# Kernel optimization log

Measured on AMD Instinct MI355X. Metric: run time of the kernel, lower is better.

The kernel has to match this reference:

```python
import jax, jax.numpy as jnp
import numpy as np

B, L, R, E, D = 16, 28, 64, 34, 512


def setup_inputs() -> dict:
    key = jax.random.key(0)
    ks = jax.random.split(key, 10)
    logits = jax.random.uniform(ks[0], (B, L, R), dtype=jnp.float32)
    evt_embeddings = jax.random.normal(ks[1], (B, 1, D), dtype=jnp.float32)
    arg_embeddings = jax.random.normal(ks[2], (B, L, D), dtype=jnp.float32)
    # valid-arg counts in [1, L] (used as mask-count multiplier and divisor)
    arg_padding_num = jax.random.randint(ks[3], (B,), 1, L + 1).astype(jnp.float32)
    evt_type_list = jax.random.randint(ks[4], (B,), 0, E)
    s = 1.0 / np.sqrt(D)
    WRT = jax.random.normal(ks[5], (R, D, D), dtype=jnp.float32) * s
    WTT = jax.random.normal(ks[6], (E, D, D), dtype=jnp.float32) * s
    w1 = jax.random.normal(ks[7], (D, 64), dtype=jnp.float32) * s
    b1 = jnp.zeros((64,), dtype=jnp.float32)
    w2 = jax.random.normal(ks[8], (64, 1), dtype=jnp.float32) * (1.0 / 8.0)
    b2 = jnp.zeros((1,), dtype=jnp.float32)
    return {"logits": logits, "evt_embeddings": evt_embeddings,
            "arg_embeddings": arg_embeddings, "arg_padding_num": arg_padding_num,
            "evt_type_list": evt_type_list, "WRT": WRT, "WTT": WTT,
            "w1": w1, "b1": b1, "w2": w2, "b2": b2}


def reference(logits, evt_embeddings, arg_embeddings, arg_padding_num,
              evt_type_list, WRT, WTT, w1, b1, w2, b2):
    # role transition matrix per (event, arg): one-hot/soft select over WRT
    # [B,L,R] x [R,D,D] -> [B,L,D,D]  (dominant, memory-bound intermediate)
    role_mats = jnp.einsum('blr,rde->blde', logits, WRT)
    # event transition matrix: one-hot select over WTT == gather
    evt_mats = WTT[evt_type_list]                      # [B,D,D]
    # event embedding transform: [B,1,D] bmm [B,D,D] -> [B,D]
    evt_trans = jnp.einsum('bd,bde->be', evt_embeddings[:, 0, :], evt_mats)
    # per-arg transform: [B,L,D] bmm [B,L,D,D] -> [B,L,D]
    role_trans = jnp.einsum('bld,blde->ble', arg_embeddings, role_mats)
    # multiply by count, sum over args, divide by count (as in the original)
    role_trans = role_trans * arg_padding_num[:, None, None]
    new_sum = jnp.sum(role_trans, axis=1)              # [B,D]
    div = new_sum / arg_padding_num[:, None]
    graph_embeddings = (div + evt_trans) / 2.0         # [B,D]
    # scorer MLP: Linear(D,64) -> ReLU -> Linear(64,1) -> Sigmoid
    h = jax.nn.relu(graph_embeddings @ w1 + b1)
    score = jax.nn.sigmoid(h @ w2 + b2)                # [B,1]
    return score
```

## Files before the change

### kernel.cpp

```cpp
#include <hip/hip_runtime.h>
#include <math.h>

#define BB 16
#define LL 28
#define RR 64
#define DD 512
#define NROLE 512
#define NEVT  256

__global__ void __launch_bounds__(256, 3) kernel_a(
    const float* __restrict__ logits,
    const float* __restrict__ arg,
    const float* __restrict__ WRT,
    const float* __restrict__ WTT,
    const float* __restrict__ evt_emb,
    const int*   __restrict__ evt_type,
    float* __restrict__ part,
    float* __restrict__ evt_part)
{
    __shared__ float smem[1024];
    const int t   = threadIdx.x;
    const int q   = blockIdx.x / 3;
    const int rem = blockIdx.x - 3 * q;

    if (rem == 2) {
        const int cid = q;
        const int b  = cid >> 4;
        const int dc = cid & 15;
        const int d0 = dc * 32;
        const int ty = evt_type[b];
        const float* Wt = WTT + (size_t)ty * DD * DD;
        const int e4 = t & 127;
        const int s  = t >> 7;
        float4 a = {0.f, 0.f, 0.f, 0.f};
#pragma unroll
        for (int db = 0; db < 32; db += 16) {
            float  em[8];
            float4 w[8];
#pragma unroll
            for (int i = 0; i < 8; ++i) {
                const int d = d0 + db + s + 2 * i;
                em[i] = evt_emb[b * DD + d];
                w[i]  = ((const float4*)(Wt + (size_t)d * DD))[e4];
            }
#pragma unroll
            for (int i = 0; i < 8; ++i) {
                a.x = fmaf(em[i], w[i].x, a.x);
                a.y = fmaf(em[i], w[i].y, a.y);
                a.z = fmaf(em[i], w[i].z, a.z);
                a.w = fmaf(em[i], w[i].w, a.w);
            }
        }
        float4* sm4 = (float4*)smem;
        if (s == 1) sm4[e4] = a;
        __syncthreads();
        if (s == 0) {
            const float4 q4 = sm4[e4];
            a.x += q4.x; a.y += q4.y; a.z += q4.z; a.w += q4.w;
            ((float4*)evt_part)[(size_t)cid * 128 + e4] = a;
        }
        return;
    }

    const int rid = 2 * q + rem;
    const int r  = rid >> 3;
    const int d0 = (rid & 7) * 64;

    const float4* Wp = (const float4*)(WRT + ((size_t)r * DD + d0) * DD);

    const int e4 = t & 127;
    const int bh = t >> 7;

    float4 w[8];
#pragma unroll
    for (int i = 0; i < 8; ++i)
        w[i] = Wp[(size_t)i * 128 + e4];

    {
        const int b  = t >> 4;
        const int d4 = t & 15;
        const float4* ap = (const float4*)(arg) + (size_t)(b * LL) * 128 + (d0 >> 2) + d4;
        const float*  lp = logits + (b * LL) * RR + r;
        float4 g = {0.f, 0.f, 0.f, 0.f};
#pragma unroll 7
        for (int l = 0; l < LL; ++l) {
            const float4 av = ap[(size_t)l * 128];
            const float lg = lp[l * RR];
            g.x = fmaf(lg, av.x, g.x);
            g.y = fmaf(lg, av.y, g.y);
            g.z = fmaf(lg, av.z, g.z);
            g.w = fmaf(lg, av.w, g.w);
        }
        smem[(4 * d4 + 0) * 16 + b] = g.x;
        smem[(4 * d4 + 1) * 16 + b] = g.y;
        smem[(4 * d4 + 2) * 16 + b] = g.z;
        smem[(4 * d4 + 3) * 16 + b] = g.w;
    }
    __syncthreads();

    float4 acc[8];
#pragma unroll
    for (int i = 0; i < 8; ++i) acc[i] = make_float4(0.f, 0.f, 0.f, 0.f);

    const float* G = smem;
    for (int kb = 0; kb < 8; ++kb) {
        const int kbn = (kb + 1) & 7;
        float4 wn[8];
#pragma unroll
        for (int i = 0; i < 8; ++i)
            wn[i] = Wp[(size_t)(kbn * 8 + i) * 128 + e4];
#pragma unroll
        for (int i = 0; i < 8; ++i) {
            const int kk = kb * 8 + i;
            const float4 ga = ((const float4*)(G + kk * 16 + 8 * bh))[0];
            const float4 gb = ((const float4*)(G + kk * 16 + 8 * bh))[1];
            acc[0].x = fmaf(ga.x, w[i].x, acc[0].x); acc[0].y = fmaf(ga.x, w[i].y, acc[0].y);
            acc[0].z = fmaf(ga.x, w[i].z, acc[0].z); acc[0].w = fmaf(ga.x, w[i].w, acc[0].w);
            acc[1].x = fmaf(ga.y, w[i].x, acc[1].x); acc[1].y = fmaf(ga.y, w[i].y, acc[1].y);
            acc[1].z = fmaf(ga.y, w[i].z, acc[1].z); acc[1].w = fmaf(ga.y, w[i].w, acc[1].w);
            acc[2].x = fmaf(ga.z, w[i].x, acc[2].x); acc[2].y = fmaf(ga.z, w[i].y, acc[2].y);
            acc[2].z = fmaf(ga.z, w[i].z, acc[2].z); acc[2].w = fmaf(ga.z, w[i].w, acc[2].w);
            acc[3].x = fmaf(ga.w, w[i].x, acc[3].x); acc[3].y = fmaf(ga.w, w[i].y, acc[3].y);
            acc[3].z = fmaf(ga.w, w[i].z, acc[3].z); acc[3].w = fmaf(ga.w, w[i].w, acc[3].w);
            acc[4].x = fmaf(gb.x, w[i].x, acc[4].x); acc[4].y = fmaf(gb.x, w[i].y, acc[4].y);
            acc[4].z = fmaf(gb.x, w[i].z, acc[4].z); acc[4].w = fmaf(gb.x, w[i].w, acc[4].w);
            acc[5].x = fmaf(gb.y, w[i].x, acc[5].x); acc[5].y = fmaf(gb.y, w[i].y, acc[5].y);
            acc[5].z = fmaf(gb.y, w[i].z, acc[5].z); acc[5].w = fmaf(gb.y, w[i].w, acc[5].w);
            acc[6].x = fmaf(gb.z, w[i].x, acc[6].x); acc[6].y = fmaf(gb.z, w[i].y, acc[6].y);
            acc[6].z = fmaf(gb.z, w[i].z, acc[6].z); acc[6].w = fmaf(gb.z, w[i].w, acc[6].w);
            acc[7].x = fmaf(gb.w, w[i].x, acc[7].x); acc[7].y = fmaf(gb.w, w[i].y, acc[7].y);
            acc[7].z = fmaf(gb.w, w[i].z, acc[7].z); acc[7].w = fmaf(gb.w, w[i].w, acc[7].w);
        }
#pragma unroll
        for (int i = 0; i < 8; ++i) w[i] = wn[i];
    }

    float4* po = (float4*)part + (size_t)rid * 2048;
#pragma unroll
    for (int i = 0; i < 8; ++i)
        po[(8 * bh + i) * 128 + e4] = acc[i];
}

__global__ void __launch_bounds__(256) kernel_reduce(
    const float* __restrict__ part,
    const float* __restrict__ evt_part,
    float* __restrict__ div_acc,
    float* __restrict__ evt_acc)
{
    const int t = threadIdx.x;
    if (blockIdx.x < 128) {
        __shared__ float4 sred[256];
        const int oo = t & 15;
        const int pg = t >> 4;
        const int o4 = blockIdx.x * 16 + oo;
        const float4* p4 = (const float4*)part;
        float4 s = {0.f, 0.f, 0.f, 0.f};
#pragma unroll 8
        for (int i = 0; i < 32; ++i) {
            const int p = pg * 32 + i;
            const float4 v = p4[(size_t)p * 2048 + o4];
            s.x += v.x; s.y += v.y; s.z += v.z; s.w += v.w;
        }
        sred[pg * 16 + oo] = s;
        __syncthreads();
        if (t < 16) {
            float4 tot = sred[t];
#pragma unroll
            for (int g = 1; g < 16; ++g) {
                const float4 v = sred[g * 16 + t];
                tot.x += v.x; tot.y += v.y; tot.z += v.z; tot.w += v.w;
            }
            ((float4*)div_acc)[blockIdx.x * 16 + t] = tot;
        }
    } else {
        const int o4 = (blockIdx.x - 128) * 256 + t;
        const int b  = o4 >> 7;
        const int el = o4 & 127;
        const float4* e4p = (const float4*)evt_part;
        float4 s = {0.f, 0.f, 0.f, 0.f};
#pragma unroll
        for (int dc = 0; dc < 16; ++dc) {
            const float4 v = e4p[(size_t)(b * 16 + dc) * 128 + el];
            s.x += v.x; s.y += v.y; s.z += v.z; s.w += v.w;
        }
        ((float4*)evt_acc)[o4] = s;
    }
}

__global__ void __launch_bounds__(256) kernel_mlp(
    const float* __restrict__ div_acc,
    const float* __restrict__ evt_acc,
    const float* __restrict__ w1,
    const float* __restrict__ b1,
    const float* __restrict__ w2,
    const float* __restrict__ b2,
    float* __restrict__ out)
{
    __shared__ float hred[256];
    const int b  = blockIdx.x;
    const int t  = threadIdx.x;
    const int j  = t & 63;
    const int dq = t >> 6;
    float hp = 0.f;
#pragma unroll 8
    for (int i = 0; i < 128; ++i) {
        const int d = dq * 128 + i;
        const float g = (div_acc[b * DD + d] + evt_acc[b * DD + d]) * 0.5f;
        hp = fmaf(g, w1[d * 64 + j], hp);
    }
    hred[t] = hp;
    __syncthreads();
    if (t < 64) {
        float h = b1[j] + hred[j] + hred[64 + j] + hred[128 + j] + hred[192 + j];
        h = fmaxf(h, 0.f);
        float v = h * w2[j];
#pragma unroll
        for (int off = 32; off > 0; off >>= 1) v += __shfl_down(v, off, 64);
        if (j == 0) out[b] = 1.f / (1.f + expf(-(v + b2[0])));
    }
}

extern "C" void kernel_launch(void* const* d_in, const int* in_sizes, int n_in,
                              void* d_out, int out_size, void* d_ws, size_t ws_size,
                              hipStream_t stream) {
    const float* logits   = (const float*)d_in[0];
    const float* evt_emb  = (const float*)d_in[1];
    const float* arg_emb  = (const float*)d_in[2];
    const int*   evt_type = (const int*)d_in[4];
    const float* WRT      = (const float*)d_in[5];
    const float* WTT      = (const float*)d_in[6];
    const float* w1       = (const float*)d_in[7];
    const float* b1       = (const float*)d_in[8];
    const float* w2       = (const float*)d_in[9];
    const float* b2       = (const float*)d_in[10];
    float* out = (float*)d_out;

    float* part     = (float*)d_ws;
    float* evt_part = part + (size_t)NROLE * 8192;
    float* div_acc  = evt_part + NEVT * DD;
    float* evt_acc  = div_acc + BB * DD;

    hipLaunchKernelGGL(kernel_a, dim3(NROLE + NEVT), dim3(256), 0, stream,
                       logits, arg_emb, WRT, WTT, evt_emb, evt_type, part, evt_part);
    hipLaunchKernelGGL(kernel_reduce, dim3(136), dim3(256), 0, stream,
                       part, evt_part, div_acc, evt_acc);
    hipLaunchKernelGGL(kernel_mlp, dim3(BB), dim3(256), 0, stream,
                       div_acc, evt_acc, w1, b1, w2, b2, out);
}
```

Baseline: 156.5 us.

## Replace partial-sum buffers and reduce kernel with direct atomic accumulation

Role and event blocks now atomically add their results into a single zeroed [B,D] buffer. This replaces writing per-block partials to workspace and summing them in a separate reduce kernel. Role work is also split across twice as many blocks, each covering half the output columns with fewer accumulators, and the occupancy hint is raised. In exchange it adds many contended float atomics and a memset launch, recomputes the logits-weighted argument sums in both column halves, and makes the summation order nondeterministic.

```diff
diff --git a/kernel.cpp b/kernel.cpp
--- a/kernel.cpp
+++ b/kernel.cpp
@@ -5,25 +5,24 @@
 #define LL 28
 #define RR 64
 #define DD 512
-#define NROLE 512
+#define NROLE 1024
 #define NEVT  256
 
-__global__ void __launch_bounds__(256, 3) kernel_a(
+__global__ void __launch_bounds__(256, 4) kernel_a(
     const float* __restrict__ logits,
     const float* __restrict__ arg,
     const float* __restrict__ WRT,
     const float* __restrict__ WTT,
     const float* __restrict__ evt_emb,
     const int*   __restrict__ evt_type,
-    float* __restrict__ part,
-    float* __restrict__ evt_part)
+    float* __restrict__ acc_buf)
 {
     __shared__ float smem[1024];
     const int t   = threadIdx.x;
-    const int q   = blockIdx.x / 3;
-    const int rem = blockIdx.x - 3 * q;
+    const int q   = blockIdx.x / 5;
+    const int rem = blockIdx.x - 5 * q;
 
-    if (rem == 2) {
+    if (rem == 4) {
         const int cid = q;
         const int b  = cid >> 4;
         const int dc = cid & 15;
@@ -57,19 +56,24 @@
         if (s == 0) {
             const float4 q4 = sm4[e4];
             a.x += q4.x; a.y += q4.y; a.z += q4.z; a.w += q4.w;
-            ((float4*)evt_part)[(size_t)cid * 128 + e4] = a;
+            float* dst = acc_buf + b * DD + e4 * 4;
+            atomicAdd(dst + 0, a.x);
+            atomicAdd(dst + 1, a.y);
+            atomicAdd(dst + 2, a.z);
+            atomicAdd(dst + 3, a.w);
         }
         return;
     }
 
-    const int rid = 2 * q + rem;
-    const int r  = rid >> 3;
-    const int d0 = (rid & 7) * 64;
+    const int rid = q * 4 + rem;
+    const int r   = rid >> 4;
+    const int d0  = ((rid >> 1) & 7) * 64;
+    const int eh  = rid & 1;
 
-    const float4* Wp = (const float4*)(WRT + ((size_t)r * DD + d0) * DD);
+    const float4* Wp = (const float4*)(WRT + ((size_t)r * DD + d0) * DD + eh * 256);
 
-    const int e4 = t & 127;
-    const int bh = t >> 7;
+    const int e4 = t & 63;
+    const int bq = t >> 6;
 
     float4 w[8];
 #pragma unroll
@@ -98,9 +102,8 @@
     }
     __syncthreads();
 
-    float4 acc[8];
-#pragma unroll
-    for (int i = 0; i < 8; ++i) acc[i] = make_float4(0.f, 0.f, 0.f, 0.f);
+    float4 acc0 = {0.f,0.f,0.f,0.f}, acc1 = {0.f,0.f,0.f,0.f};
+    float4 acc2 = {0.f,0.f,0.f,0.f}, acc3 = {0.f,0.f,0.f,0.f};
 
     const float* G = smem;
     for (int kb = 0; kb < 8; ++kb) {
@@ -112,84 +115,33 @@
 #pragma unroll
         for (int i = 0; i < 8; ++i) {
             const int kk = kb * 8 + i;
-            const float4 ga = ((const float4*)(G + kk * 16 + 8 * bh))[0];
-            const float4 gb = ((const float4*)(G + kk * 16 + 8 * bh))[1];
-            acc[0].x = fmaf(ga.x, w[i].x, acc[0].x); acc[0].y = fmaf(ga.x, w[i].y, acc[0].y);
-            acc[0].z = fmaf(ga.x, w[i].z, acc[0].z); acc[0].w = fmaf(ga.x, w[i].w, acc[0].w);
-            acc[1].x = fmaf(ga.y, w[i].x, acc[1].x); acc[1].y = fmaf(ga.y, w[i].y, acc[1].y);
-            acc[1].z = fmaf(ga.y, w[i].z, acc[1].z); acc[1].w = fmaf(ga.y, w[i].w, acc[1].w);
-            acc[2].x = fmaf(ga.z, w[i].x, acc[2].x); acc[2].y = fmaf(ga.z, w[i].y, acc[2].y);
-            acc[2].z = fmaf(ga.z, w[i].z, acc[2].z); acc[2].w = fmaf(ga.z, w[i].w, acc[2].w);
-            acc[3].x = fmaf(ga.w, w[i].x, acc[3].x); acc[3].y = fmaf(ga.w, w[i].y, acc[3].y);
-            acc[3].z = fmaf(ga.w, w[i].z, acc[3].z); acc[3].w = fmaf(ga.w, w[i].w, acc[3].w);
-            acc[4].x = fmaf(gb.x, w[i].x, acc[4].x); acc[4].y = fmaf(gb.x, w[i].y, acc[4].y);
-            acc[4].z = fmaf(gb.x, w[i].z, acc[4].z); acc[4].w = fmaf(gb.x, w[i].w, acc[4].w);
-            acc[5].x = fmaf(gb.y, w[i].x, acc[5].x); acc[5].y = fmaf(gb.y, w[i].y, acc[5].y);
-            acc[5].z = fmaf(gb.y, w[i].z, acc[5].z); acc[5].w = fmaf(gb.y, w[i].w, acc[5].w);
-            acc[6].x = fmaf(gb.z, w[i].x, acc[6].x); acc[6].y = fmaf(gb.z, w[i].y, acc[6].y);
-            acc[6].z = fmaf(gb.z, w[i].z, acc[6].z); acc[6].w = fmaf(gb.z, w[i].w, acc[6].w);
-            acc[7].x = fmaf(gb.w, w[i].x, acc[7].x); acc[7].y = fmaf(gb.w, w[i].y, acc[7].y);
-            acc[7].z = fmaf(gb.w, w[i].z, acc[7].z); acc[7].w = fmaf(gb.w, w[i].w, acc[7].w);
+            const float4 ga = ((const float4*)(G + kk * 16 + 4 * bq))[0];
+            acc0.x = fmaf(ga.x, w[i].x, acc0.x); acc0.y = fmaf(ga.x, w[i].y, acc0.y);
+            acc0.z = fmaf(ga.x, w[i].z, acc0.z); acc0.w = fmaf(ga.x, w[i].w, acc0.w);
+            acc1.x = fmaf(ga.y, w[i].x, acc1.x); acc1.y = fmaf(ga.y, w[i].y, acc1.y);
+            acc1.z = fmaf(ga.y, w[i].z, acc1.z); acc1.w = fmaf(ga.y, w[i].w, acc1.w);
+            acc2.x = fmaf(ga.z, w[i].x, acc2.x); acc2.y = fmaf(ga.z, w[i].y, acc2.y);
+            acc2.z = fmaf(ga.z, w[i].z, acc2.z); acc2.w = fmaf(ga.z, w[i].w, acc2.w);
+            acc3.x = fmaf(ga.w, w[i].x, acc3.x); acc3.y = fmaf(ga.w, w[i].y, acc3.y);
+            acc3.z = fmaf(ga.w, w[i].z, acc3.z); acc3.w = fmaf(ga.w, w[i].w, acc3.w);
         }
 #pragma unroll
         for (int i = 0; i < 8; ++i) w[i] = wn[i];
     }
 
-    float4* po = (float4*)part + (size_t)rid * 2048;
-#pragma unroll
-    for (int i = 0; i < 8; ++i)
-        po[(8 * bh + i) * 128 + e4] = acc[i];
-}
-
-__global__ void __launch_bounds__(256) kernel_reduce(
-    const float* __restrict__ part,
-    const float* __restrict__ evt_part,
-    float* __restrict__ div_acc,
-    float* __restrict__ evt_acc)
-{
-    const int t = threadIdx.x;
-    if (blockIdx.x < 128) {
-        __shared__ float4 sred[256];
-        const int oo = t & 15;
-        const int pg = t >> 4;
-        const int o4 = blockIdx.x * 16 + oo;
-        const float4* p4 = (const float4*)part;
-        float4 s = {0.f, 0.f, 0.f, 0.f};
-#pragma unroll 8
-        for (int i = 0; i < 32; ++i) {
-            const int p = pg * 32 + i;
-            const float4 v = p4[(size_t)p * 2048 + o4];
-            s.x += v.x; s.y += v.y; s.z += v.z; s.w += v.w;
-        }
-        sred[pg * 16 + oo] = s;
-        __syncthreads();
-        if (t < 16) {
-            float4 tot = sred[t];
-#pragma unroll
-            for (int g = 1; g < 16; ++g) {
-                const float4 v = sred[g * 16 + t];
-                tot.x += v.x; tot.y += v.y; tot.z += v.z; tot.w += v.w;
-            }
-            ((float4*)div_acc)[blockIdx.x * 16 + t] = tot;
-        }
-    } else {
-        const int o4 = (blockIdx.x - 128) * 256 + t;
-        const int b  = o4 >> 7;
-        const int el = o4 & 127;
-        const float4* e4p = (const float4*)evt_part;
-        float4 s = {0.f, 0.f, 0.f, 0.f};
-#pragma unroll
-        for (int dc = 0; dc < 16; ++dc) {
-            const float4 v = e4p[(size_t)(b * 16 + dc) * 128 + el];
-            s.x += v.x; s.y += v.y; s.z += v.z; s.w += v.w;
-        }
-        ((float4*)evt_acc)[o4] = s;
-    }
+    float* dst = acc_buf + (4 * bq) * DD + eh * 256 + e4 * 4;
+    atomicAdd(dst + 0,          acc0.x); atomicAdd(dst + 1,          acc0.y);
+    atomicAdd(dst + 2,          acc0.z); atomicAdd(dst + 3,          acc0.w);
+    atomicAdd(dst + DD + 0,     acc1.x); atomicAdd(dst + DD + 1,     acc1.y);
+    atomicAdd(dst + DD + 2,     acc1.z); atomicAdd(dst + DD + 3,     acc1.w);
+    atomicAdd(dst + 2 * DD + 0, acc2.x); atomicAdd(dst + 2 * DD + 1, acc2.y);
+    atomicAdd(dst + 2 * DD + 2, acc2.z); atomicAdd(dst + 2 * DD + 3, acc2.w);
+    atomicAdd(dst + 3 * DD + 0, acc3.x); atomicAdd(dst + 3 * DD + 1, acc3.y);
+    atomicAdd(dst + 3 * DD + 2, acc3.z); atomicAdd(dst + 3 * DD + 3, acc3.w);
 }
 
 __global__ void __launch_bounds__(256) kernel_mlp(
-    const float* __restrict__ div_acc,
-    const float* __restrict__ evt_acc,
+    const float* __restrict__ acc_buf,
     const float* __restrict__ w1,
     const float* __restrict__ b1,
     const float* __restrict__ w2,
@@ -205,7 +157,7 @@
 #pragma unroll 8
     for (int i = 0; i < 128; ++i) {
         const int d = dq * 128 + i;
-        const float g = (div_acc[b * DD + d] + evt_acc[b * DD + d]) * 0.5f;
+        const float g = acc_buf[b * DD + d] * 0.5f;
         hp = fmaf(g, w1[d * 64 + j], hp);
     }
     hred[t] = hp;
@@ -235,15 +187,12 @@
     const float* b2       = (const float*)d_in[10];
     float* out = (float*)d_out;
 
-    float* part     = (float*)d_ws;
-    float* evt_part = part + (size_t)NROLE * 8192;
-    float* div_acc  = evt_part + NEVT * DD;
-    float* evt_acc  = div_acc + BB * DD;
+    float* acc_buf = (float*)d_ws;
+
+    hipMemsetAsync(acc_buf, 0, BB * DD * sizeof(float), stream);
 
     hipLaunchKernelGGL(kernel_a, dim3(NROLE + NEVT), dim3(256), 0, stream,
-                       logits, arg_emb, WRT, WTT, evt_emb, evt_type, part, evt_part);
-    hipLaunchKernelGGL(kernel_reduce, dim3(136), dim3(256), 0, stream,
-                       part, evt_part, div_acc, evt_acc);
+                       logits, arg_emb, WRT, WTT, evt_emb, evt_type, acc_buf);
     hipLaunchKernelGGL(kernel_mlp, dim3(BB), dim3(256), 0, stream,
-                       div_acc, evt_acc, w1, b1, w2, b2, out);
+                       acc_buf, w1, b1, w2, b2, out);
 }
```

New measurement: 196.5 us. 25.6% more time.

## Precompute logit-weighted arg sums in separate kernel and retile role GEMV

Applied to the files above, without the earlier changes.

Moves the per-role weighted sum of argument embeddings (G = sum_l logits*arg) into a new kernel that writes it once to workspace in a [k][b] layout, so the role blocks no longer recompute it redundantly. The role kernel is retiled: each block covers 128 k rows and half the output columns, split across four waves that reduce through shared memory. It now reads G from global memory per k and streams WRT without the explicit double buffer. Partial outputs drop from 512 to 256 slices, so the reduce kernel sums fewer partials, at the cost of an extra launch and a 2 MB G write/read.

```diff
diff --git a/kernel.cpp b/kernel.cpp
--- a/kernel.cpp
+++ b/kernel.cpp
@@ -5,26 +5,46 @@
 #define LL 28
 #define RR 64
 #define DD 512
+#define KK (RR * DD)
 #define NROLE 512
 #define NEVT  256
 
-__global__ void __launch_bounds__(256, 3) kernel_a(
+__global__ void __launch_bounds__(512) kernel_g(
     const float* __restrict__ logits,
     const float* __restrict__ arg,
+    float* __restrict__ Gt)
+{
+    const int b  = blockIdx.x >> 5;
+    const int rp = blockIdx.x & 31;
+    const int r0 = rp * 2;
+    const int d  = threadIdx.x;
+    const float* lp  = logits + (b * LL) * RR;
+    const float* apb = arg + (size_t)(b * LL) * DD + d;
+    float g0 = 0.f, g1 = 0.f;
+#pragma unroll
+    for (int l = 0; l < LL; ++l) {
+        const float av = apb[(size_t)l * DD];
+        g0 = fmaf(lp[l * RR + r0],     av, g0);
+        g1 = fmaf(lp[l * RR + r0 + 1], av, g1);
+    }
+    Gt[((size_t)r0 * DD + d) * 16 + b]       = g0;
+    Gt[((size_t)(r0 + 1) * DD + d) * 16 + b] = g1;
+}
+
+__global__ void __launch_bounds__(256, 3) kernel_a(
     const float* __restrict__ WRT,
     const float* __restrict__ WTT,
     const float* __restrict__ evt_emb,
     const int*   __restrict__ evt_type,
+    const float* __restrict__ Gt,
     float* __restrict__ part,
     float* __restrict__ evt_part)
 {
-    __shared__ float smem[1024];
-    const int t   = threadIdx.x;
-    const int q   = blockIdx.x / 3;
-    const int rem = blockIdx.x - 3 * q;
-
-    if (rem == 2) {
-        const int cid = q;
+    __shared__ float4 comb[1024];
+    const int t = threadIdx.x;
+
+    if (blockIdx.x >= NROLE) {
+        const int cid = blockIdx.x - NROLE;
         const int b  = cid >> 4;
         const int dc = cid & 15;
         const int d0 = dc * 32;
@@ -51,94 +71,69 @@
                 a.w = fmaf(em[i], w[i].w, a.w);
             }
         }
-        float4* sm4 = (float4*)smem;
-        if (s == 1) sm4[e4] = a;
+        if (s == 1) comb[e4] = a;
         __syncthreads();
         if (s == 0) {
-            const float4 q4 = sm4[e4];
+            const float4 q4 = comb[e4];
             a.x += q4.x; a.y += q4.y; a.z += q4.z; a.w += q4.w;
             ((float4*)evt_part)[(size_t)cid * 128 + e4] = a;
         }
         return;
     }
 
-    const int rid = 2 * q + rem;
-    const int r  = rid >> 3;
-    const int d0 = (rid & 7) * 64;
-
-    const float4* Wp = (const float4*)(WRT + ((size_t)r * DD + d0) * DD);
-
-    const int e4 = t & 127;
-    const int bh = t >> 7;
-
-    float4 w[8];
-#pragma unroll
-    for (int i = 0; i < 8; ++i)
-        w[i] = Wp[(size_t)i * 128 + e4];
-
-    {
-        const int b  = t >> 4;
-        const int d4 = t & 15;
-        const float4* ap = (const float4*)(arg) + (size_t)(b * LL) * 128 + (d0 >> 2) + d4;
-        const float*  lp = logits + (b * LL) * RR + r;
-        float4 g = {0.f, 0.f, 0.f, 0.f};
-#pragma unroll 7
-        for (int l = 0; l < LL; ++l) {
-            const float4 av = ap[(size_t)l * 128];
-            const float lg = lp[l * RR];
-            g.x = fmaf(lg, av.x, g.x);
-            g.y = fmaf(lg, av.y, g.y);
-            g.z = fmaf(lg, av.z, g.z);
-            g.w = fmaf(lg, av.w, g.w);
-        }
-        smem[(4 * d4 + 0) * 16 + b] = g.x;
-        smem[(4 * d4 + 1) * 16 + b] = g.y;
-        smem[(4 * d4 + 2) * 16 + b] = g.z;
-        smem[(4 * d4 + 3) * 16 + b] = g.w;
+    const int c  = blockIdx.x >> 1;
+    const int eh = blockIdx.x & 1;
+    const int e4 = t & 63;
+    const int wid = __builtin_amdgcn_readfirstlane(t >> 6);
+    const int bh = wid & 1;
+    const int rg = wid >> 1;
+    const int k0 = __builtin_amdgcn_readfirstlane(c * 128 + rg * 64);
+
+    const float4* Wp = (const float4*)WRT + (size_t)k0 * 128 + eh * 64 + e4;
+    const float*  Gp = Gt + (size_t)k0 * 16 + bh * 8;
+
+    float4 acc[8];
+#pragma unroll
+    for (int j = 0; j < 8; ++j) acc[j] = make_float4(0.f, 0.f, 0.f, 0.f);
+
+#pragma unroll 8
+    for (int i = 0; i < 64; ++i) {
+        const float4 w = Wp[(size_t)i * 128];
+        const float* gr = Gp + i * 16;
+        const float g0 = gr[0], g1 = gr[1], g2 = gr[2], g3 = gr[3];
+        const float g4 = gr[4], g5 = gr[5], g6 = gr[6], g7 = gr[7];
+        acc[0].x = fmaf(g0, w.x, acc[0].x); acc[0].y = fmaf(g0, w.y, acc[0].y);
+        acc[0].z = fmaf(g0, w.z, acc[0].z); acc[0].w = fmaf(g0, w.w, acc[0].w);
+        acc[1].x = fmaf(g1, w.x, acc[1].x); acc[1].y = fmaf(g1, w.y, acc[1].y);
+        acc[1].z = fmaf(g1, w.z, acc[1].z); acc[1].w = fmaf(g1, w.w, acc[1].w);
+        acc[2].x = fmaf(g2, w.x, acc[2].x); acc[2].y = fmaf(g2, w.y, acc[2].y);
+        acc[2].z = fmaf(g2, w.z, acc[2].z); acc[2].w = fmaf(g2, w.w, acc[2].w);
+        acc[3].x = fmaf(g3, w.x, acc[3].x); acc[3].y = fmaf(g3, w.y, acc[3].y);
+        acc[3].z = fmaf(g3, w.z, acc[3].z); acc[3].w = fmaf(g3, w.w, acc[3].w);
+        acc[4].x = fmaf(g4, w.x, acc[4].x); acc[4].y = fmaf(g4, w.y, acc[4].y);
+        acc[4].z = fmaf(g4, w.z, acc[4].z); acc[4].w = fmaf(g4, w.w, acc[4].w);
+        acc[5].x = fmaf(g5, w.x, acc[5].x); acc[5].y = fmaf(g5, w.y, acc[5].y);
+        acc[5].z = fmaf(g5, w.z, acc[5].z); acc[5].w = fmaf(g5, w.w, acc[5].w);
+        acc[6].x = fmaf(g6, w.x, acc[6].x); acc[6].y = fmaf(g6, w.y, acc[6].y);
+        acc[6].z = fmaf(g6, w.z, acc[6].z); acc[6].w = fmaf(g6, w.w, acc[6].w);
+        acc[7].x = fmaf(g7, w.x, acc[7].x); acc[7].y = fmaf(g7, w.y, acc[7].y);
+        acc[7].z = fmaf(g7, w.z, acc[7].z); acc[7].w = fmaf(g7, w.w, acc[7].w);
+    }
+
+    if (rg == 1) {
+#pragma unroll
+        for (int j = 0; j < 8; ++j) comb[(bh * 8 + j) * 64 + e4] = acc[j];
     }
     __syncthreads();
-
-    float4 acc[8];
-#pragma unroll
-    for (int i = 0; i < 8; ++i) acc[i] = make_float4(0.f, 0.f, 0.f, 0.f);
-
-    const float* G = smem;
-    for (int kb = 0; kb < 8; ++kb) {
-        const int kbn = (kb + 1) & 7;
-        float4 wn[8];
-#pragma unroll
-        for (int i = 0; i < 8; ++i)
-            wn[i] = Wp[(size_t)(kbn * 8 + i) * 128 + e4];
-#pragma unroll
-        for (int i = 0; i < 8; ++i) {
-            const int kk = kb * 8 + i;
-            const float4 ga = ((const float4*)(G + kk * 16 + 8 * bh))[0];
-            const float4 gb = ((const float4*)(G + kk * 16 + 8 * bh))[1];
-            acc[0].x = fmaf(ga.x, w[i].x, acc[0].x); acc[0].y = fmaf(ga.x, w[i].y, acc[0].y);
-            acc[0].z = fmaf(ga.x, w[i].z, acc[0].z); acc[0].w = fmaf(ga.x, w[i].w, acc[0].w);
-            acc[1].x = fmaf(ga.y, w[i].x, acc[1].x); acc[1].y = fmaf(ga.y, w[i].y, acc[1].y);
-            acc[1].z = fmaf(ga.y, w[i].z, acc[1].z); acc[1].w = fmaf(ga.y, w[i].w, acc[1].w);
-            acc[2].x = fmaf(ga.z, w[i].x, acc[2].x); acc[2].y = fmaf(ga.z, w[i].y, acc[2].y);
-            acc[2].z = fmaf(ga.z, w[i].z, acc[2].z); acc[2].w = fmaf(ga.z, w[i].w, acc[2].w);
-            acc[3].x = fmaf(ga.w, w[i].x, acc[3].x); acc[3].y = fmaf(ga.w, w[i].y, acc[3].y);
-            acc[3].z = fmaf(ga.w, w[i].z, acc[3].z); acc[3].w = fmaf(ga.w, w[i].w, acc[3].w);
-            acc[4].x = fmaf(gb.x, w[i].x, acc[4].x); acc[4].y = fmaf(gb.x, w[i].y, acc[4].y);
-            acc[4].z = fmaf(gb.x, w[i].z, acc[4].z); acc[4].w = fmaf(gb.x, w[i].w, acc[4].w);
-            acc[5].x = fmaf(gb.y, w[i].x, acc[5].x); acc[5].y = fmaf(gb.y, w[i].y, acc[5].y);
-            acc[5].z = fmaf(gb.y, w[i].z, acc[5].z); acc[5].w = fmaf(gb.y, w[i].w, acc[5].w);
-            acc[6].x = fmaf(gb.z, w[i].x, acc[6].x); acc[6].y = fmaf(gb.z, w[i].y, acc[6].y);
-            acc[6].z = fmaf(gb.z, w[i].z, acc[6].z); acc[6].w = fmaf(gb.z, w[i].w, acc[6].w);
-            acc[7].x = fmaf(gb.w, w[i].x, acc[7].x); acc[7].y = fmaf(gb.w, w[i].y, acc[7].y);
-            acc[7].z = fmaf(gb.w, w[i].z, acc[7].z); acc[7].w = fmaf(gb.w, w[i].w, acc[7].w);
-        }
-#pragma unroll
-        for (int i = 0; i < 8; ++i) w[i] = wn[i];
-    }
-
-    float4* po = (float4*)part + (size_t)rid * 2048;
-#pragma unroll
-    for (int i = 0; i < 8; ++i)
-        po[(8 * bh + i) * 128 + e4] = acc[i];
+    if (rg == 0) {
+        float4* po = (float4*)part + (size_t)c * 2048;
+#pragma unroll
+        for (int j = 0; j < 8; ++j) {
+            const float4 q = comb[(bh * 8 + j) * 64 + e4];
+            acc[j].x += q.x; acc[j].y += q.y; acc[j].z += q.z; acc[j].w += q.w;
+            po[(bh * 8 + j) * 128 + eh * 64 + e4] = acc[j];
+        }
+    }
 }
 
 __global__ void __launch_bounds__(256) kernel_reduce(
@@ -155,9 +150,9 @@
         const int o4 = blockIdx.x * 16 + oo;
         const float4* p4 = (const float4*)part;
         float4 s = {0.f, 0.f, 0.f, 0.f};
-#pragma unroll 8
-        for (int i = 0; i < 32; ++i) {
-            const int p = pg * 32 + i;
+#pragma unroll 4
+        for (int i = 0; i < 16; ++i) {
+            const int p = pg * 16 + i;
             const float4 v = p4[(size_t)p * 2048 + o4];
             s.x += v.x; s.y += v.y; s.z += v.z; s.w += v.w;
         }
@@ -235,13 +230,16 @@
     const float* b2       = (const float*)d_in[10];
     float* out = (float*)d_out;
 
-    float* part     = (float*)d_ws;
-    float* evt_part = part + (size_t)NROLE * 8192;
+    float* Gt       = (float*)d_ws;
+    float* part     = Gt + (size_t)KK * 16;
+    float* evt_part = part + (size_t)256 * 8192;
     float* div_acc  = evt_part + NEVT * DD;
     float* evt_acc  = div_acc + BB * DD;
 
+    hipLaunchKernelGGL(kernel_g, dim3(512), dim3(512), 0, stream,
+                       logits, arg_emb, Gt);
     hipLaunchKernelGGL(kernel_a, dim3(NROLE + NEVT), dim3(256), 0, stream,
-                       logits, arg_emb, WRT, WTT, evt_emb, evt_type, part, evt_part);
+                       WRT, WTT, evt_emb, evt_type, Gt, part, evt_part);
     hipLaunchKernelGGL(kernel_reduce, dim3(136), dim3(256), 0, stream,
                        part, evt_part, div_acc, evt_acc);
     hipLaunchKernelGGL(kernel_mlp, dim3(BB), dim3(256), 0, stream,
```

Result: no change. 159.3 us (+1.8%).
